# Performance work log

Hardware: AMD Instinct MI355X
Metric: run time of the kernel (lower is better)

## Reference

```python
import jax, jax.numpy as jnp
import numpy as np

B, T, C = 4, 2048, 1024
N_HEADS = 16
HEAD_DIM = C // N_HEADS


def setup_inputs() -> dict:
    key = jax.random.key(0)
    k1, k2, k3, k4, k5 = jax.random.split(key, 5)
    x = jax.random.normal(k1, (B, T, C), dtype=jnp.float32)
    # torch Linear: y = x @ W.T + b; store W as [out, in]
    w_qkv = jax.random.normal(k2, (3 * C, C), dtype=jnp.float32) * (1.0 / np.sqrt(C))
    b_qkv = jax.random.normal(k3, (3 * C,), dtype=jnp.float32) * 0.01
    w_proj = jax.random.normal(k4, (C, C), dtype=jnp.float32) * (1.0 / np.sqrt(C))
    b_proj = jax.random.normal(k5, (C,), dtype=jnp.float32) * 0.01
    return {"x": x, "w_qkv": w_qkv, "b_qkv": b_qkv, "w_proj": w_proj, "b_proj": b_proj}


def reference(x, w_qkv, b_qkv, w_proj, b_proj):
    Bx, Tx, Cx = x.shape
    scale = 1.0 / np.sqrt(HEAD_DIM)
    qkv = x @ w_qkv.T + b_qkv                              # [B,T,3C]
    qkv = qkv.reshape(Bx, Tx, 3, N_HEADS, HEAD_DIM)
    qkv = jnp.transpose(qkv, (2, 0, 3, 1, 4))              # [3,B,H,T,D]
    q, k, v = qkv[0], qkv[1], qkv[2]
    att = jnp.einsum('bhqd,bhkd->bhqk', q, k) * scale      # [B,H,T,T]
    causal = jnp.tril(jnp.ones((Tx, Tx), dtype=bool))
    att = jnp.where(causal[None, None, :, :], att, -jnp.inf)
    att = jax.nn.softmax(att, axis=-1)
    # dropout p=0.0 (eval) -> identity
    out = jnp.einsum('bhqk,bhkd->bhqd', att, v)            # [B,H,T,D]
    out = jnp.transpose(out, (0, 2, 1, 3)).reshape(Bx, Tx, Cx)
    return out @ w_proj.T + b_proj
```

## Files before the change

### kernel.cpp

```cpp
#include <hip/hip_runtime.h>
#include <hip/hip_bf16.h>
#include <cstdint>

typedef __attribute__((ext_vector_type(8))) short bf16x8;
typedef __attribute__((ext_vector_type(4))) float f32x4;
typedef __attribute__((ext_vector_type(16))) float f32x16;

#define MFMA16(a, b, c) __builtin_amdgcn_mfma_f32_16x16x32_bf16(a, b, c, 0, 0, 0)
#define MFMA32(a, b, c) __builtin_amdgcn_mfma_f32_32x32x16_bf16(a, b, c, 0, 0, 0)

typedef __attribute__((address_space(1))) uint32_t as1_u32;
typedef __attribute__((address_space(3))) uint32_t as3_u32;
static __device__ __forceinline__ void gload16(const void* g, void* l) {
  __builtin_amdgcn_global_load_lds((as1_u32*)g, (as3_u32*)l, 16, 0, 0);
}

static __device__ __forceinline__ ushort f2b(float f) {
  union { float f; uint32_t u; } v; v.f = f;
  uint32_t u = v.u;
  uint32_t r = (u + 0x7FFFu + ((u >> 16) & 1u)) >> 16;
  return (ushort)r;
}

static __device__ __forceinline__ uint32_t cvtpk(float a, float b) {
  uint32_t r;
  asm("v_cvt_pk_bf16_f32 %0, %1, %2" : "=v"(r) : "v"(a), "v"(b));
  return r;
}
static __device__ __forceinline__ void plswap(uint32_t& a, uint32_t& b) {
  asm volatile("v_permlane32_swap_b32 %0, %1" : "+v"(a), "+v"(b));
}

#define QSCALE 0.1803368782f

__global__ void cvt_f32_bf16(const float* __restrict__ in, ushort* __restrict__ out, int n4) {
  int i = blockIdx.x * blockDim.x + threadIdx.x;
  if (i >= n4) return;
  const float4 v = ((const float4*)in)[i];
  ushort4 o;
  o.x = f2b(v.x); o.y = f2b(v.y); o.z = f2b(v.z); o.w = f2b(v.w);
  ((ushort4*)out)[i] = o;
}

template<int EPI>
__global__ __launch_bounds__(256) void gemm_bt(
    const ushort* __restrict__ A,
    const ushort* __restrict__ W,
    const float* __restrict__ bias,
    int M, int N, int K,
    ushort* __restrict__ q_ws, ushort* __restrict__ k_ws, ushort* __restrict__ v_ws,
    float* __restrict__ out) {
  __shared__ ushort As[128 * 64];
  __shared__ ushort Bs[128 * 64];
  const int tid = threadIdx.x;
  const int m0 = blockIdx.y * 128, n0 = blockIdx.x * 128;
  const int lane = tid & 63, w = tid >> 6;
  const int lr = lane & 15, lg = lane >> 4;
  const int wm = (w >> 1) * 64, wn = (w & 1) * 64;
  f32x4 acc[4][4] = {};

  for (int k0 = 0; k0 < K; k0 += 64) {
    __syncthreads();
#pragma unroll
    for (int it = 0; it < 4; ++it) {
      const int chunk = it * 256 + tid;
      const int r = chunk >> 3;
      const int c = (chunk & 7) * 8;
      gload16(&A[(size_t)(m0 + r) * K + k0 + c], &As[chunk * 8]);
      gload16(&W[(size_t)(n0 + r) * K + k0 + c], &Bs[chunk * 8]);
    }
    __syncthreads();
#pragma unroll
    for (int kk = 0; kk < 2; ++kk) {
      bf16x8 a[4], b[4];
#pragma unroll
      for (int mi = 0; mi < 4; ++mi)
        a[mi] = *(const bf16x8*)&As[(wm + mi * 16 + lr) * 64 + kk * 32 + lg * 8];
#pragma unroll
      for (int ni = 0; ni < 4; ++ni)
        b[ni] = *(const bf16x8*)&Bs[(wn + ni * 16 + lr) * 64 + kk * 32 + lg * 8];
#pragma unroll
      for (int mi = 0; mi < 4; ++mi)
#pragma unroll
        for (int ni = 0; ni < 4; ++ni)
          acc[mi][ni] = MFMA16(a[mi], b[ni], acc[mi][ni]);
    }
  }

#pragma unroll
  for (int mi = 0; mi < 4; ++mi) {
#pragma unroll
    for (int ni = 0; ni < 4; ++ni) {
      const int rowb = m0 + wm + mi * 16 + lg * 4;
      const int col = n0 + wn + ni * 16 + lr;
      float v[4];
#pragma unroll
      for (int i = 0; i < 4; ++i) v[i] = acc[mi][ni][i] + bias[col];
      if (EPI == 0) {
        const int sel = col >> 10;
        const int rem = col & 1023;
        const int h = rem >> 6, d = rem & 63;
        const int bb = rowb >> 11, t0 = rowb & 2047;
        if (sel == 2) {
          ushort4 st;
          st.x = f2b(v[0]); st.y = f2b(v[1]); st.z = f2b(v[2]); st.w = f2b(v[3]);
          *(ushort4*)&v_ws[((size_t)(bb * 16 + h) * 64 + d) * 2048 + t0] = st;
        } else if (sel == 0) {
#pragma unroll
          for (int i = 0; i < 4; ++i)
            q_ws[((size_t)(bb * 16 + h) * 2048 + t0 + i) * 64 + d] = f2b(v[i] * QSCALE);
        } else {
#pragma unroll
          for (int i = 0; i < 4; ++i)
            k_ws[((size_t)(bb * 16 + h) * 2048 + t0 + i) * 64 + d] = f2b(v[i]);
        }
      } else {
#pragma unroll
        for (int i = 0; i < 4; ++i)
          out[(size_t)(rowb + i) * N + col] = v[i];
      }
    }
  }
}

__global__ __launch_bounds__(256) void attn_v5(
    const ushort* __restrict__ Q, const ushort* __restrict__ K,
    const ushort* __restrict__ VT, ushort* __restrict__ O ) {
  const int blk = blockIdx.x;
  const int bh = blk & 63;
  const int pr = blk >> 6;
  const int tid = threadIdx.x;
  const int w = tid >> 6, lane = tid & 63;
  const int l31 = lane & 31, l5 = lane >> 5;
  const int bb = bh >> 4, h = bh & 15;
  const size_t base = (size_t)bh * 2048 * 64;
  const ushort* Qb = Q + base;
  const ushort* Kb = K + base;
  const ushort* VTb = VT + base;

  __shared__ ushort Ks[2][64 * 64];
  __shared__ ushort Vs[2][64 * 64];
  __shared__ float l_lds[4][32];

#define STAGE(buf, kt_)                                              \
  do {                                                               \
    const ushort* Kt = Kb + (size_t)(kt_) * 64 * 64;                 \
    const ushort* Vt = VTb + (kt_) * 64;                             \
    _Pragma("unroll") for (int i_ = 0; i_ < 2; ++i_) {               \
      const int ch = i_ * 256 + tid;                                 \
      const int r = ch >> 3;                                         \
      const int csw = ((ch & 7) ^ (r & 7)) * 8;                      \
      gload16(&Kt[(size_t)r * 64 + csw], &Ks[buf][ch * 8]);          \
      gload16(&Vt[(size_t)r * 2048 + csw], &Vs[buf][ch * 8]);        \
    }                                                                \
  } while (0)

#pragma unroll 1
  for (int ph = 0; ph < 2; ++ph) {
    const int s = ph ? pr : 15 - pr;
    const int q0w = s * 128 + w * 32;
    const int nt = 2 * s + 2;
    const int qlane = q0w + l31;

    bf16x8 qf[4];
#pragma unroll
    for (int dblk = 0; dblk < 4; ++dblk)
      qf[dblk] = *(const bf16x8*)&Qb[(size_t)qlane * 64 + dblk * 16 + l5 * 8];

    f32x16 o0 = {}, o1 = {};
    float lsum = 0.f;

    STAGE(0, 0);
    __syncthreads();

    for (int kt = 0; kt < nt; ++kt) {
      const int cur = kt & 1;
      if (kt + 1 < nt) STAGE(cur ^ 1, kt + 1);
      const int k0 = kt << 6;
      const ushort* Ksc = Ks[cur];
      const ushort* Vsc = Vs[cur];
#pragma unroll
      for (int kblk = 0; kblk < 2; ++kblk) {
        const int kbase = k0 + kblk * 32;
        if (kbase <= q0w + 31) {
          f32x16 st = {};
          __builtin_amdgcn_s_setprio(1);
#pragma unroll
          for (int dblk = 0; dblk < 4; ++dblk) {
            const int row = kblk * 32 + l31;
            bf16x8 ka = *(const bf16x8*)&Ksc[row * 64 + (((dblk * 2 + l5) ^ (row & 7)) * 8)];
            st = MFMA32(ka, qf[dblk], st);
          }
          __builtin_amdgcn_s_setprio(0);
          if (kbase + 31 > q0w) {
#pragma unroll
            for (int r = 0; r < 16; ++r) {
              const int kk = kbase + (r & 3) + 8 * (r >> 2) + 4 * l5;
              st[r] = (kk <= qlane) ? st[r] : -INFINITY;
            }
          }
          float p[16];
#pragma unroll
          for (int r = 0; r < 16; ++r) {
            p[r] = __builtin_amdgcn_exp2f(st[r]);
            lsum += p[r];
          }
#pragma unroll
          for (int sbl = 0; sbl < 2; ++sbl) {
            uint32_t P0 = cvtpk(p[8 * sbl + 0], p[8 * sbl + 1]);
            uint32_t P1 = cvtpk(p[8 * sbl + 2], p[8 * sbl + 3]);
            uint32_t P2 = cvtpk(p[8 * sbl + 4], p[8 * sbl + 5]);
            uint32_t P3 = cvtpk(p[8 * sbl + 6], p[8 * sbl + 7]);
            plswap(P0, P2);
            plswap(P1, P3);
            union { uint32_t u[4]; bf16x8 v; } pk;
            pk.u[0] = P0; pk.u[1] = P1; pk.u[2] = P2; pk.u[3] = P3;
            const int kchunk = kblk * 4 + sbl * 2 + l5;
            __builtin_amdgcn_s_setprio(1);
#pragma unroll
            for (int db2 = 0; db2 < 2; ++db2) {
              const int vrow = db2 * 32 + l31;
              bf16x8 vb = *(const bf16x8*)&Vsc[vrow * 64 + ((kchunk ^ (vrow & 7)) * 8)];
              if (db2 == 0) o0 = MFMA32(pk.v, vb, o0);
              else          o1 = MFMA32(pk.v, vb, o1);
            }
            __builtin_amdgcn_s_setprio(0);
          }
        }
      }
      __syncthreads();
    }

    const float lfull = lsum + __shfl_xor(lsum, 32);
    if (lane < 32) l_lds[w][lane] = 1.f / lfull;
#pragma unroll
    for (int r = 0; r < 16; ++r) {
      const int qoff = (r & 3) + 8 * (r >> 2) + 4 * l5;
      const float inv = l_lds[w][qoff];
      const int t = q0w + qoff;
      ushort* op = &O[(size_t)(bb * 2048 + t) * 1024 + h * 64 + l31];
      op[0] = f2b(o0[r] * inv);
      op[32] = f2b(o1[r] * inv);
    }
  }
#undef STAGE
}

extern "C" void kernel_launch(void* const* d_in, const int* in_sizes, int n_in,
                              void* d_out, int out_size, void* d_ws, size_t ws_size,
                              hipStream_t stream) {
  const float* x = (const float*)d_in[0];
  const float* w_qkv = (const float*)d_in[1];
  const float* b_qkv = (const float*)d_in[2];
  const float* w_proj = (const float*)d_in[3];
  const float* b_proj = (const float*)d_in[4];
  float* out = (float*)d_out;

  char* ws = (char*)d_ws;
  const size_t SZ_X = (size_t)8192 * 1024 * 2;
  const size_t SZ_WQ = (size_t)3072 * 1024 * 2;
  const size_t SZ_WP = (size_t)1024 * 1024 * 2;
  ushort* xb = (ushort*)(ws);
  ushort* wqb = (ushort*)(ws + SZ_X);
  ushort* wpb = (ushort*)(ws + SZ_X + SZ_WQ);
  ushort* q_ws = (ushort*)(ws + SZ_X + SZ_WQ + SZ_WP);
  ushort* k_ws = q_ws + (size_t)8192 * 1024;
  ushort* v_ws = k_ws + (size_t)8192 * 1024;

  cvt_f32_bf16<<<8388608 / 4 / 256, 256, 0, stream>>>(x, xb, 8388608 / 4);
  cvt_f32_bf16<<<3145728 / 4 / 256, 256, 0, stream>>>(w_qkv, wqb, 3145728 / 4);
  cvt_f32_bf16<<<1048576 / 4 / 256, 256, 0, stream>>>(w_proj, wpb, 1048576 / 4);

  gemm_bt<0><<<dim3(3072 / 128, 8192 / 128), 256, 0, stream>>>(
      xb, wqb, b_qkv, 8192, 3072, 1024, q_ws, k_ws, v_ws, nullptr);

  attn_v5<<<512, 256, 0, stream>>>(q_ws, k_ws, v_ws, xb);

  gemm_bt<1><<<dim3(1024 / 128, 8192 / 128), 256, 0, stream>>>(
      xb, wpb, b_proj, 8192, 1024, 1024, nullptr, nullptr, nullptr, out);
}
```

Measured before the change: 187.4 us.

## Pipeline GEMM k-loop with 4-stage LDS ring, XOR swizzle and XCD remap

After: 183.9 us. About the same (-1.9%).

```diff
diff --git a/kernel.cpp b/kernel.cpp
--- a/kernel.cpp
+++ b/kernel.cpp
@@ -50,42 +50,73 @@
     int M, int N, int K,
     ushort* __restrict__ q_ws, ushort* __restrict__ k_ws, ushort* __restrict__ v_ws,
     float* __restrict__ out) {
-  __shared__ ushort As[128 * 64];
-  __shared__ ushort Bs[128 * 64];
+  __shared__ ushort As[4][64 * 64];
+  __shared__ ushort Bs[4][64 * 64];
   const int tid = threadIdx.x;
-  const int m0 = blockIdx.y * 128, n0 = blockIdx.x * 128;
+  const int nbx = N >> 7;
+  const int cpx = gridDim.x >> 3;
+  const int wg = (blockIdx.x & 7) * cpx + (blockIdx.x >> 3);
+  const int m0 = (wg / nbx) * 128, n0 = (wg % nbx) * 128;
   const int lane = tid & 63, w = tid >> 6;
   const int lr = lane & 15, lg = lane >> 4;
   const int wm = (w >> 1) * 64, wn = (w & 1) * 64;
   f32x4 acc[4][4] = {};
 
-  for (int k0 = 0; k0 < K; k0 += 64) {
-    __syncthreads();
-#pragma unroll
-    for (int it = 0; it < 4; ++it) {
-      const int chunk = it * 256 + tid;
-      const int r = chunk >> 3;
-      const int c = (chunk & 7) * 8;
-      gload16(&A[(size_t)(m0 + r) * K + k0 + c], &As[chunk * 8]);
-      gload16(&W[(size_t)(n0 + r) * K + k0 + c], &Bs[chunk * 8]);
-    }
-    __syncthreads();
-#pragma unroll
-    for (int kk = 0; kk < 2; ++kk) {
-      bf16x8 a[4], b[4];
-#pragma unroll
-      for (int mi = 0; mi < 4; ++mi)
-        a[mi] = *(const bf16x8*)&As[(wm + mi * 16 + lr) * 64 + kk * 32 + lg * 8];
+  const int nt = K >> 5;
+
+#define GSTAGE(buf_, kt_)                                                   \
+  do {                                                                      \
+    const ushort* Asrc = A + (size_t)m0 * K + (kt_) * 32;                   \
+    const ushort* Bsrc = W + (size_t)n0 * K + (kt_) * 32;                   \
+    _Pragma("unroll") for (int i_ = 0; i_ < 2; ++i_) {                      \
+      const int ch = i_ * 256 + tid;                            \
+      const int prow = ch >> 3, pchk = ch & 7;                              \
+      const int lchk = pchk ^ (prow & 7);              \
+      const int r = prow * 2 + (lchk >> 2), kc = (lchk & 3) * 8;            \
+      gload16(&Asrc[(size_t)r * K + kc], &As[buf_][ch * 8]);                \
+      gload16(&Bsrc[(size_t)r * K + kc], &Bs[buf_][ch * 8]);                \
+    }                                                                       \
+  } while (0)
+
+  GSTAGE(0, 0);
+  GSTAGE(1, 1);
+  GSTAGE(2, 2);
+  asm volatile("s_waitcnt vmcnt(8)" ::: "memory");
+  __builtin_amdgcn_s_barrier();
+  asm volatile("" ::: "memory");
+
+  for (int t = 0; t < nt; ++t) {
+    if (t + 3 < nt) GSTAGE((t + 3) & 3, t + 3);
+    const ushort* Asc = As[t & 3];
+    const ushort* Bsc = Bs[t & 3];
+    bf16x8 a[4], b[4];
+#pragma unroll
+    for (int mi = 0; mi < 4; ++mi) {
+      const int r = wm + mi * 16 + lr;
+      a[mi] = *(const bf16x8*)&Asc[(r >> 1) * 64 + (((((r & 1) << 2) | lg) ^ ((r >> 1) & 7)) * 8)];
+    }
+#pragma unroll
+    for (int ni = 0; ni < 4; ++ni) {
+      const int r = wn + ni * 16 + lr;
+      b[ni] = *(const bf16x8*)&Bsc[(r >> 1) * 64 + (((((r & 1) << 2) | lg) ^ ((r >> 1) & 7)) * 8)];
+    }
+    __builtin_amdgcn_s_setprio(1);
+#pragma unroll
+    for (int mi = 0; mi < 4; ++mi)
 #pragma unroll
       for (int ni = 0; ni < 4; ++ni)
-        b[ni] = *(const bf16x8*)&Bs[(wn + ni * 16 + lr) * 64 + kk * 32 + lg * 8];
-#pragma unroll
-      for (int mi = 0; mi < 4; ++mi)
-#pragma unroll
-        for (int ni = 0; ni < 4; ++ni)
-          acc[mi][ni] = MFMA16(a[mi], b[ni], acc[mi][ni]);
-    }
+        acc[mi][ni] = MFMA16(a[mi], b[ni], acc[mi][ni]);
+    __builtin_amdgcn_s_setprio(0);
+    if (t + 3 < nt)
+      asm volatile("s_waitcnt vmcnt(8)" ::: "memory");
+    else if (t + 2 < nt)
+      asm volatile("s_waitcnt vmcnt(4)" ::: "memory");
+    else if (t + 1 < nt)
+      asm volatile("s_waitcnt vmcnt(0)" ::: "memory");
+    __builtin_amdgcn_s_barrier();
+    asm volatile("" ::: "memory");
   }
+#undef GSTAGE
 
 #pragma unroll
   for (int mi = 0; mi < 4; ++mi) {
@@ -271,11 +302,11 @@
   cvt_f32_bf16<<<3145728 / 4 / 256, 256, 0, stream>>>(w_qkv, wqb, 3145728 / 4);
   cvt_f32_bf16<<<1048576 / 4 / 256, 256, 0, stream>>>(w_proj, wpb, 1048576 / 4);
 
-  gemm_bt<0><<<dim3(3072 / 128, 8192 / 128), 256, 0, stream>>>(
+  gemm_bt<0><<<1536, 256, 0, stream>>>(
       xb, wqb, b_qkv, 8192, 3072, 1024, q_ws, k_ws, v_ws, nullptr);
 
   attn_v5<<<512, 256, 0, stream>>>(q_ws, k_ws, v_ws, xb);
 
-  gemm_bt<1><<<dim3(1024 / 128, 8192 / 128), 256, 0, stream>>>(
+  gemm_bt<1><<<512, 256, 0, stream>>>(
       xb, wpb, b_proj, 8192, 1024, 1024, nullptr, nullptr, nullptr, out);
 }
```
